# Kernel tuning notes

Hardware: AMD Instinct MI355X
Metric: run time of the kernel (lower is better)

Reference implementation:

```python
import jax, jax.numpy as jnp
import numpy as np
import math

DIM = 1024
H = 16
HD = DIM // H  # 64
M = 64         # num_features
B, S = 4, 4096


def setup_inputs() -> dict:
    key = jax.random.key(0)
    ks = jax.random.split(key, 10)
    sc = 1.0 / math.sqrt(DIM)
    return {
        "x": jax.random.normal(ks[0], (B, S, DIM), dtype=jnp.float32),
        "Wq": jax.random.normal(ks[1], (DIM, DIM), dtype=jnp.float32) * sc,
        "bq": jax.random.normal(ks[2], (DIM,), dtype=jnp.float32) * 0.01,
        "Wk": jax.random.normal(ks[3], (DIM, DIM), dtype=jnp.float32) * sc,
        "bk": jax.random.normal(ks[4], (DIM,), dtype=jnp.float32) * 0.01,
        "Wv": jax.random.normal(ks[5], (DIM, DIM), dtype=jnp.float32) * sc,
        "bv": jax.random.normal(ks[6], (DIM,), dtype=jnp.float32) * 0.01,
        "Wo": jax.random.normal(ks[7], (DIM, DIM), dtype=jnp.float32) * sc,
        "bo": jax.random.normal(ks[8], (DIM,), dtype=jnp.float32) * 0.01,
        "P": jax.random.normal(ks[9], (H, M, HD), dtype=jnp.float32),
    }


def _feature_map(t, P):
    # t: [b,h,s,d], P: [h,m,d] -> relu(t @ P^T) / sqrt(m)
    proj = jnp.einsum("bhsd,hmd->bhsm", t, P)
    return jax.nn.relu(proj) * (1.0 / math.sqrt(P.shape[1]))


def reference(x, Wq, bq, Wk, bk, Wv, bv, Wo, bo, P):
    b, s, dim = x.shape
    h, m, hd = P.shape
    # Linear projections (torch Linear: x @ W^T + b), split heads -> [b,h,s,hd]
    def split_heads(y):
        return y.reshape(b, s, h, hd).transpose(0, 2, 1, 3)
    q = split_heads(x @ Wq.T + bq)
    k = split_heads(x @ Wk.T + bk)
    v = split_heads(x @ Wv.T + bv)
    q_prime = _feature_map(q, P)  # [b,h,s,m]
    k_prime = _feature_map(k, P)  # [b,h,s,m]
    kv = jnp.einsum("bhsm,bhsd->bhmd", k_prime, v)       # [b,h,m,hd]
    attn = jnp.einsum("bhsm,bhmd->bhsd", q_prime, kv)    # [b,h,s,hd]
    attn = attn.transpose(0, 2, 1, 3).reshape(b, s, dim)
    return attn @ Wo.T + bo
```

## Files before the change

kernel.cpp:

```cpp
#include <hip/hip_runtime.h>
#include <hip/hip_bf16.h>
#include <cstdint>

typedef __bf16 bf16_t;
typedef bf16_t bf16x8 __attribute__((ext_vector_type(8)));
typedef float f32x4 __attribute__((ext_vector_type(4)));
typedef float f32x16 __attribute__((ext_vector_type(16)));


__device__ __forceinline__ void gload_lds16(const bf16_t* g, bf16_t* l) {
  __builtin_amdgcn_global_load_lds(
      (const __attribute__((address_space(1))) uint32_t*)g,
      (__attribute__((address_space(3))) uint32_t*)l, 16, 0, 0);
}

__global__ void prep_misc(const float* __restrict__ x, const float* __restrict__ Wv,
                          const float* __restrict__ bv,
                          bf16_t* __restrict__ xb, bf16_t* __restrict__ WvO,
                          float* __restrict__ bcat) {
  int b = blockIdx.x, t = threadIdx.x;
  if (b < 8192) {
    long i = (long)b * 256 + t;
    const f32x4* p = (const f32x4*)(x + i * 8);
    f32x4 a = p[0], c = p[1];
    bf16x8 o;
#pragma unroll
    for (int j = 0; j < 4; ++j) { o[j] = (bf16_t)a[j]; o[j + 4] = (bf16_t)c[j]; }
    *(bf16x8*)(xb + i * 8) = o;
  } else if (b < 8704) {
    long i = (long)(b - 8192) * 256 + t;
    const f32x4* p = (const f32x4*)(Wv + i * 8);
    f32x4 a = p[0], c = p[1];
    bf16x8 o;
#pragma unroll
    for (int j = 0; j < 4; ++j) { o[j] = (bf16_t)a[j]; o[j + 4] = (bf16_t)c[j]; }
    *(bf16x8*)(WvO + i * 8) = o;
  } else {
    *(f32x4*)&bcat[2048 + t * 4] = *(const f32x4*)&bv[t * 4];
  }
}

__global__ __launch_bounds__(256) void prep_wqk(
    const float* __restrict__ Wq, const float* __restrict__ bq,
    const float* __restrict__ Wk, const float* __restrict__ bk,
    const float* __restrict__ P,
    bf16_t* __restrict__ Wcat, float* __restrict__ bcat)
{
  int bid = blockIdx.x;
  int qk = bid >> 7, h = (bid >> 3) & 15, kt = bid & 7;
  const float* W = qk ? Wk : Wq;
  const float* bias = qk ? bk : bq;
  __shared__ float Pl[64 * 64];
  __shared__ float Wlt[128 * 68];
  int t = threadIdx.x;
  int k0 = kt * 128;
  for (int i = t * 4; i < 4096; i += 1024)
    *(f32x4*)&Pl[i] = *(const f32x4*)&P[h * 4096 + i];
  for (int fi = t; fi < 2048; fi += 256) {
    int row = fi >> 5;
    int c4 = fi & 31;
    f32x4 w = *(const f32x4*)&W[(long)(h * 64 + row) * 1024 + k0 + c4 * 4];
#pragma unroll
    for (int j = 0; j < 4; ++j) Wlt[(c4 * 4 + j) * 68 + row] = w[j];
  }
  __syncthreads();
  int kloc = t >> 1;
  int mh = (t & 1) * 32;
  for (int m = mh; m < mh + 32; ++m) {
    f32x4 s = {0.f, 0.f, 0.f, 0.f};
#pragma unroll
    for (int dd = 0; dd < 16; ++dd)
      s += (*(const f32x4*)&Pl[m * 64 + dd * 4]) * (*(const f32x4*)&Wlt[kloc * 68 + dd * 4]);
    float a = s[0] + s[1] + s[2] + s[3];
    Wcat[(long)(qk * 1024 + h * 64 + m) * 1024 + k0 + kloc] = (bf16_t)a;
  }
  if (kt == 0 && t < 64) {
    float a = 0.f;
    for (int d = 0; d < 64; ++d) a += Pl[t * 64 + d] * bias[h * 64 + d];
    bcat[qk * 1024 + h * 64 + t] = a;
  }
}

template <int EPI>
__global__ __launch_bounds__(512, 2) void gemm256(
    const bf16_t* __restrict__ A, int lda,
    const bf16_t* __restrict__ B0, int ldb,
    const float* __restrict__ bias,
    void* __restrict__ Cv, int ldc,
    int K, int ncols, int cpx,
    int rows_per_batch, long bstride)
{
  __shared__ bf16_t sA[2][16384];
  __shared__ bf16_t sB[2][16384];

  const int lin = blockIdx.x;
  const int wgid = (lin & 7) * cpx + (lin >> 3);
  const int row0 = (wgid / ncols) * 256;
  const int col0 = (wgid % ncols) * 256;

  const int tid = threadIdx.x;
  const int w = tid >> 6, l = tid & 63;
  const int wr = w >> 2, wc = w & 3;
  const int l31 = l & 31, kh = l >> 5, x7 = l & 7;

  const bf16_t* Bm = B0 + (long)(row0 / rows_per_batch) * bstride;

  long a_off[4], b_off[4];
#pragma unroll
  for (int i = 0; i < 4; ++i) {
    int c = i * 512 + tid;
    int r = c >> 3;
    int kqs = (c & 7) ^ (r & 7);
    a_off[i] = (long)(row0 + r) * lda + kqs * 8;
    b_off[i] = (long)(col0 + r) * ldb + kqs * 8;
  }
  const int ldst = tid * 8;

  const int abase = (wr * 128 + l31) * 64;
  const int bbase = (wc * 64 + l31) * 64;
  const int e0 = ((0 + kh) ^ x7) * 8;
  const int e1 = ((2 + kh) ^ x7) * 8;
  const int e2 = ((4 + kh) ^ x7) * 8;
  const int e3 = ((6 + kh) ^ x7) * 8;

  f32x16 acc[4][2] = {};
  const int NT = K >> 6;

#pragma unroll
  for (int i = 0; i < 4; ++i) {
    gload_lds16(A + a_off[i], &sA[0][i * 4096 + ldst]);
    gload_lds16(Bm + b_off[i], &sB[0][i * 4096 + ldst]);
  }
  __syncthreads();

#define TILE_BODY(PC, PN, T)                                                            \
  {                                                                                     \
    bf16x8 afr[4][2], bfr[2][2];                                                        \
    _Pragma("unroll") for (int mi = 0; mi < 4; ++mi) {                                  \
      afr[mi][0] = *(const bf16x8*)&sA[PC][abase + mi * 2048 + e0];                     \
      afr[mi][1] = *(const bf16x8*)&sA[PC][abase + mi * 2048 + e1];                     \
    }                                                                                   \
    _Pragma("unroll") for (int ni = 0; ni < 2; ++ni) {                                  \
      bfr[ni][0] = *(const bf16x8*)&sB[PC][bbase + ni * 2048 + e0];                     \
      bfr[ni][1] = *(const bf16x8*)&sB[PC][bbase + ni * 2048 + e1];                     \
    }                                                                                   \
    if ((T) + 1 < NT) {                                                                 \
      long ks = (long)((T) + 1) * 64;                                                   \
      _Pragma("unroll") for (int i = 0; i < 4; ++i) {                                   \
        gload_lds16(A + a_off[i] + ks, &sA[PN][i * 4096 + ldst]);                       \
        gload_lds16(Bm + b_off[i] + ks, &sB[PN][i * 4096 + ldst]);                      \
      }                                                                                 \
    }                                                                                   \
    __builtin_amdgcn_s_setprio(1);                                                      \
    _Pragma("unroll") for (int mi = 0; mi < 4; ++mi)                                    \
      _Pragma("unroll") for (int ni = 0; ni < 2; ++ni) {                                \
        acc[mi][ni] = __builtin_amdgcn_mfma_f32_32x32x16_bf16(afr[mi][0], bfr[ni][0], acc[mi][ni], 0, 0, 0); \
        acc[mi][ni] = __builtin_amdgcn_mfma_f32_32x32x16_bf16(afr[mi][1], bfr[ni][1], acc[mi][ni], 0, 0, 0); \
      }                                                                                 \
    __builtin_amdgcn_s_setprio(0);                                                      \
    _Pragma("unroll") for (int mi = 0; mi < 4; ++mi) {                                  \
      afr[mi][0] = *(const bf16x8*)&sA[PC][abase + mi * 2048 + e2];                     \
      afr[mi][1] = *(const bf16x8*)&sA[PC][abase + mi * 2048 + e3];                     \
    }                                                                                   \
    _Pragma("unroll") for (int ni = 0; ni < 2; ++ni) {                                  \
      bfr[ni][0] = *(const bf16x8*)&sB[PC][bbase + ni * 2048 + e2];                     \
      bfr[ni][1] = *(const bf16x8*)&sB[PC][bbase + ni * 2048 + e3];                     \
    }                                                                                   \
    __builtin_amdgcn_s_setprio(1);                                                      \
    _Pragma("unroll") for (int mi = 0; mi < 4; ++mi)                                    \
      _Pragma("unroll") for (int ni = 0; ni < 2; ++ni) {                                \
        acc[mi][ni] = __builtin_amdgcn_mfma_f32_32x32x16_bf16(afr[mi][0], bfr[ni][0], acc[mi][ni], 0, 0, 0); \
        acc[mi][ni] = __builtin_amdgcn_mfma_f32_32x32x16_bf16(afr[mi][1], bfr[ni][1], acc[mi][ni], 0, 0, 0); \
      }                                                                                 \
    __builtin_amdgcn_s_setprio(0);                                                      \
    __syncthreads();                                                                    \
  }

  for (int t = 0; t < NT; t += 2) {
    TILE_BODY(0, 1, t);
    TILE_BODY(1, 0, t + 1);
  }
#undef TILE_BODY

#pragma unroll
  for (int ni = 0; ni < 2; ++ni) {
    const int gcol = col0 + wc * 64 + ni * 32 + l31;
    const float bz = bias[gcol];
    const bool doRelu = (EPI == 1) && (gcol < 2048);
#pragma unroll
    for (int mi = 0; mi < 4; ++mi) {
      const int rbase = row0 + wr * 128 + mi * 32 + 4 * kh;
#pragma unroll
      for (int reg = 0; reg < 16; ++reg) {
        const int grow = rbase + (reg & 3) + 8 * (reg >> 2);
        float v = acc[mi][ni][reg] + bz;
        if constexpr (EPI == 1) { if (doRelu) v = fmaxf(v, 0.f) * 0.125f; }
        if constexpr (EPI == 2)
          ((float*)Cv)[(long)grow * ldc + gcol] = v;
        else
          ((bf16_t*)Cv)[(long)grow * ldc + gcol] = (bf16_t)v;
      }
    }
  }
}

__global__ __launch_bounds__(512, 4) void gemm128(
    const bf16_t* __restrict__ A, int lda,
    const bf16_t* __restrict__ B0, int ldb,
    const float* __restrict__ bias,
    float* __restrict__ C, int ldc,
    int K, int ncols, int cpx,
    int rows_per_batch, long bstride)
{
  __shared__ bf16_t sA[2][8192];
  __shared__ bf16_t sB[2][8192];

  const int lin = blockIdx.x;
  const int wgid = (lin & 7) * cpx + (lin >> 3);
  const int row0 = (wgid / ncols) * 128;
  const int col0 = (wgid % ncols) * 128;

  const int tid = threadIdx.x;
  const int w = tid >> 6, l = tid & 63;
  const int wr = w >> 2, wc = w & 3;
  const int l31 = l & 31, kh = l >> 5, x7 = l & 7;

  const bf16_t* Bm = B0 + (long)(row0 / rows_per_batch) * bstride;

  long a_off[2], b_off[2];
#pragma unroll
  for (int i = 0; i < 2; ++i) {
    int c = i * 512 + tid;
    int r = c >> 3;
    int kqs = (c & 7) ^ (r & 7);
    a_off[i] = (long)(row0 + r) * lda + kqs * 8;
    b_off[i] = (long)(col0 + r) * ldb + kqs * 8;
  }
  const int ldst = tid * 8;

  const int abase = (wr * 64 + l31) * 64;
  const int bbase = (wc * 32 + l31) * 64;
  const int e0 = ((0 + kh) ^ x7) * 8;
  const int e1 = ((2 + kh) ^ x7) * 8;
  const int e2 = ((4 + kh) ^ x7) * 8;
  const int e3 = ((6 + kh) ^ x7) * 8;

  f32x16 acc[2] = {};
  const int NT = K >> 6;

#pragma unroll
  for (int i = 0; i < 2; ++i) {
    gload_lds16(A + a_off[i], &sA[0][i * 4096 + ldst]);
    gload_lds16(Bm + b_off[i], &sB[0][i * 4096 + ldst]);
  }
  __syncthreads();

#define TILE128(PC, PN, T)                                                              \
  {                                                                                     \
    bf16x8 afr[2][2], bfr[2];                                                           \
    _Pragma("unroll") for (int mi = 0; mi < 2; ++mi) {                                  \
      afr[mi][0] = *(const bf16x8*)&sA[PC][abase + mi * 2048 + e0];                     \
      afr[mi][1] = *(const bf16x8*)&sA[PC][abase + mi * 2048 + e1];                     \
    }                                                                                   \
    bfr[0] = *(const bf16x8*)&sB[PC][bbase + e0];                                       \
    bfr[1] = *(const bf16x8*)&sB[PC][bbase + e1];                                       \
    if ((T) + 1 < NT) {                                                                 \
      long ks = (long)((T) + 1) * 64;                                                   \
      _Pragma("unroll") for (int i = 0; i < 2; ++i) {                                   \
        gload_lds16(A + a_off[i] + ks, &sA[PN][i * 4096 + ldst]);                       \
        gload_lds16(Bm + b_off[i] + ks, &sB[PN][i * 4096 + ldst]);                      \
      }                                                                                 \
    }                                                                                   \
    __builtin_amdgcn_s_setprio(1);                                                      \
    _Pragma("unroll") for (int mi = 0; mi < 2; ++mi) {                                  \
      acc[mi] = __builtin_amdgcn_mfma_f32_32x32x16_bf16(afr[mi][0], bfr[0], acc[mi], 0, 0, 0); \
      acc[mi] = __builtin_amdgcn_mfma_f32_32x32x16_bf16(afr[mi][1], bfr[1], acc[mi], 0, 0, 0); \
    }                                                                                   \
    __builtin_amdgcn_s_setprio(0);                                                      \
    _Pragma("unroll") for (int mi = 0; mi < 2; ++mi) {                                  \
      afr[mi][0] = *(const bf16x8*)&sA[PC][abase + mi * 2048 + e2];                     \
      afr[mi][1] = *(const bf16x8*)&sA[PC][abase + mi * 2048 + e3];                     \
    }                                                                                   \
    bfr[0] = *(const bf16x8*)&sB[PC][bbase + e2];                                       \
    bfr[1] = *(const bf16x8*)&sB[PC][bbase + e3];                                       \
    __builtin_amdgcn_s_setprio(1);                                                      \
    _Pragma("unroll") for (int mi = 0; mi < 2; ++mi) {                                  \
      acc[mi] = __builtin_amdgcn_mfma_f32_32x32x16_bf16(afr[mi][0], bfr[0], acc[mi], 0, 0, 0); \
      acc[mi] = __builtin_amdgcn_mfma_f32_32x32x16_bf16(afr[mi][1], bfr[1], acc[mi], 0, 0, 0); \
    }                                                                                   \
    __builtin_amdgcn_s_setprio(0);                                                      \
    __syncthreads();                                                                    \
  }

  for (int t = 0; t < NT; t += 2) {
    TILE128(0, 1, t);
    TILE128(1, 0, t + 1);
  }
#undef TILE128

  const int gcol = col0 + wc * 32 + l31;
  const float bz = bias[gcol];
#pragma unroll
  for (int mi = 0; mi < 2; ++mi) {
    const int rbase = row0 + wr * 64 + mi * 32 + 4 * kh;
#pragma unroll
    for (int reg = 0; reg < 16; ++reg) {
      const int grow = rbase + (reg & 3) + 8 * (reg >> 2);
      C[(long)grow * ldc + gcol] = acc[mi][reg] + bz;
    }
  }
}

__global__ __launch_bounds__(256) void kv_partial(
    const bf16_t* __restrict__ QKV, float* __restrict__ kvpart)
{
  int bh = blockIdx.x;
  int split = blockIdx.y;
  int b = bh >> 4, h = bh & 15;
  __shared__ alignas(16) bf16_t Kt[64 * 32];
  __shared__ alignas(16) bf16_t Vt[64 * 32];
  int t = threadIdx.x;
  int wv = t >> 6, lane = t & 63, lhi = lane >> 4, llo = lane & 15;
  int r = t >> 3;
  int c = (t & 7) * 8;
  f32x4 acc[4] = {};
  long rowbase = ((long)b * 4096 + split * 512) * 3072 + h * 64 + c;
  for (int sc = 0; sc < 16; ++sc) {
    long off = rowbase + (long)(sc * 32 + r) * 3072;
    bf16x8 kk = *(const bf16x8*)(QKV + off + 1024);
    bf16x8 vvv = *(const bf16x8*)(QKV + off + 2048);
#pragma unroll
    for (int j = 0; j < 8; ++j) {
      Kt[(c + j) * 32 + r] = kk[j];
      Vt[(c + j) * 32 + r] = vvv[j];
    }
    __syncthreads();
    bf16x8 a = *(const bf16x8*)&Kt[(wv * 16 + llo) * 32 + lhi * 8];
#pragma unroll
    for (int ni = 0; ni < 4; ++ni) {
      bf16x8 bb = *(const bf16x8*)&Vt[(ni * 16 + llo) * 32 + lhi * 8];
      acc[ni] = __builtin_amdgcn_mfma_f32_16x16x32_bf16(a, bb, acc[ni], 0, 0, 0);
    }
    __syncthreads();
  }
#pragma unroll
  for (int ni = 0; ni < 4; ++ni)
#pragma unroll
    for (int j = 0; j < 4; ++j) {
      int m = wv * 16 + lhi * 4 + j;
      int d = ni * 16 + llo;
      kvpart[((long)split * 64 + bh) * 4096 + m * 64 + d] = acc[ni][j];
    }
}

__global__ void kv_reduce(const float* __restrict__ part, float* __restrict__ kv) {
  int i = blockIdx.x * 256 + threadIdx.x;
  float s = 0.f;
#pragma unroll
  for (int sp = 0; sp < 8; ++sp) s += part[sp * 262144 + i];
  kv[i] = s;
}

__global__ __launch_bounds__(256) void wcombt_kernel(
    const float* __restrict__ kv, const float* __restrict__ Wo,
    bf16_t* __restrict__ WcT)
{
  int nt = blockIdx.x, h = blockIdx.y, b = blockIdx.z;
  __shared__ float kvs[4096];
  int t = threadIdx.x;
  for (int i = t * 4; i < 4096; i += 1024)
    *(f32x4*)&kvs[i] = *(const f32x4*)&kv[((long)b * 16 + h) * 4096 + i];
  __syncthreads();
  int n = nt * 128 + (t >> 1);
  int mh = (t & 1) * 32;
  f32x4 wo[16];
#pragma unroll
  for (int dd = 0; dd < 16; ++dd) wo[dd] = *(const f32x4*)&Wo[(long)n * 1024 + h * 64 + dd * 4];
  for (int m = mh; m < mh + 32; ++m) {
    f32x4 s = {0.f, 0.f, 0.f, 0.f};
#pragma unroll
    for (int dd = 0; dd < 16; ++dd)
      s += (*(const f32x4*)&kvs[m * 64 + dd * 4]) * wo[dd];
    WcT[((long)b * 1024 + n) * 1024 + h * 64 + m] = (bf16_t)(s[0] + s[1] + s[2] + s[3]);
  }
}

extern "C" void kernel_launch(void* const* d_in, const int* in_sizes, int n_in,
                              void* d_out, int out_size, void* d_ws, size_t ws_size,
                              hipStream_t stream) {
  (void)in_sizes; (void)n_in; (void)out_size; (void)ws_size;
  const float* x  = (const float*)d_in[0];
  const float* Wq = (const float*)d_in[1];
  const float* bq = (const float*)d_in[2];
  const float* Wk = (const float*)d_in[3];
  const float* bk = (const float*)d_in[4];
  const float* Wv = (const float*)d_in[5];
  const float* bv = (const float*)d_in[6];
  const float* Wo = (const float*)d_in[7];
  const float* bo = (const float*)d_in[8];
  const float* P  = (const float*)d_in[9];
  float* out = (float*)d_out;

  char* ws = (char*)d_ws;
  bf16_t* xb     = (bf16_t*)(ws + 0);
  bf16_t* QKV    = (bf16_t*)(ws + 33554432);
  bf16_t* Wcat   = (bf16_t*)(ws + 134217728);
  float*  bcat   = (float*) (ws + 140509184);
  float*  kvpart = (float*) (ws + 140521472);
  float*  kvbuf  = (float*) (ws + 148910080);
  bf16_t* WcT    = (bf16_t*)(ws + 149958656);

  prep_misc<<<8705, 256, 0, stream>>>(x, Wv, bv, xb, Wcat + (size_t)2048 * 1024, bcat);
  prep_wqk<<<256, 256, 0, stream>>>(Wq, bq, Wk, bk, P, Wcat, bcat);

  gemm256<1><<<768, 512, 0, stream>>>(
      xb, 1024, Wcat, 1024, bcat, QKV, 3072, 1024, 12, 96, 1 << 30, 0);

  kv_partial<<<dim3(64, 8), 256, 0, stream>>>(QKV, kvpart);
  kv_reduce<<<1024, 256, 0, stream>>>(kvpart, kvbuf);

  wcombt_kernel<<<dim3(8, 16, 4), 256, 0, stream>>>(kvbuf, Wo, WcT);

  gemm128<<<1024, 512, 0, stream>>>(
      QKV, 3072, WcT, 1024, bo, out, 1024, 1024, 8, 128, 4096, (long)1024 * 1024);
}
```

Before: 232.4 us.

## Store LDS tiles in MFMA fragment order instead of XOR-swizzled rows

Both GEMM kernels now stage global tiles into shared memory so that each wave's MFMA operand fragment is a contiguous 64-lane run of 16-byte chunks. The per-lane XOR swizzle and its address arithmetic go away, and LDS reads become linear, conflict-free vector loads. The cost moves to global loads: each thread now fetches 16-byte pieces spread across rows with strided k offsets, which may reduce coalescing per wavefront.

```diff
diff --git a/kernel.cpp b/kernel.cpp
--- a/kernel.cpp
+++ b/kernel.cpp
@@ -101,27 +101,30 @@
   const int tid = threadIdx.x;
   const int w = tid >> 6, l = tid & 63;
   const int wr = w >> 2, wc = w & 3;
-  const int l31 = l & 31, kh = l >> 5, x7 = l & 7;
+  const int l31 = l & 31, kh = l >> 5;
+  const int lofs = l * 8;
 
   const bf16_t* Bm = B0 + (long)(row0 / rows_per_batch) * bstride;
 
   long a_off[4], b_off[4];
 #pragma unroll
-  for (int i = 0; i < 4; ++i) {
-    int c = i * 512 + tid;
-    int r = c >> 3;
-    int kqs = (c & 7) ^ (r & 7);
-    a_off[i] = (long)(row0 + r) * lda + kqs * 8;
-    b_off[i] = (long)(col0 + r) * ldb + kqs * 8;
+  for (int j = 0; j < 4; ++j) {
+    int c = j * 512 + tid;
+    int h = c >> 10;
+    int cr = c & 1023;
+    int s = cr >> 8;
+    int mi = (cr >> 6) & 3;
+    int khs = (cr >> 5) & 1;
+    int r31 = cr & 31;
+    int row = h * 128 + mi * 32 + r31;
+    int kk = s * 16 + khs * 8;
+    a_off[j] = (long)(row0 + row) * lda + kk;
+    b_off[j] = (long)(col0 + row) * ldb + kk;
   }
   const int ldst = tid * 8;
 
-  const int abase = (wr * 128 + l31) * 64;
-  const int bbase = (wc * 64 + l31) * 64;
-  const int e0 = ((0 + kh) ^ x7) * 8;
-  const int e1 = ((2 + kh) ^ x7) * 8;
-  const int e2 = ((4 + kh) ^ x7) * 8;
-  const int e3 = ((6 + kh) ^ x7) * 8;
+  const int abase = wr * 8192 + lofs;
+  const int bbase = (wc >> 1) * 8192 + (wc & 1) * 1024 + lofs;
 
   f32x16 acc[4][2] = {};
   const int NT = K >> 6;
@@ -137,12 +140,12 @@
   {                                                                                     \
     bf16x8 afr[4][2], bfr[2][2];                                                        \
     _Pragma("unroll") for (int mi = 0; mi < 4; ++mi) {                                  \
-      afr[mi][0] = *(const bf16x8*)&sA[PC][abase + mi * 2048 + e0];                     \
-      afr[mi][1] = *(const bf16x8*)&sA[PC][abase + mi * 2048 + e1];                     \
+      afr[mi][0] = *(const bf16x8*)&sA[PC][abase + mi * 512];                           \
+      afr[mi][1] = *(const bf16x8*)&sA[PC][abase + 2048 + mi * 512];                    \
     }                                                                                   \
     _Pragma("unroll") for (int ni = 0; ni < 2; ++ni) {                                  \
-      bfr[ni][0] = *(const bf16x8*)&sB[PC][bbase + ni * 2048 + e0];                     \
-      bfr[ni][1] = *(const bf16x8*)&sB[PC][bbase + ni * 2048 + e1];                     \
+      bfr[ni][0] = *(const bf16x8*)&sB[PC][bbase + ni * 512];                           \
+      bfr[ni][1] = *(const bf16x8*)&sB[PC][bbase + 2048 + ni * 512];                    \
     }                                                                                   \
     if ((T) + 1 < NT) {                                                                 \
       long ks = (long)((T) + 1) * 64;                                                   \
@@ -159,12 +162,12 @@
       }                                                                                 \
     __builtin_amdgcn_s_setprio(0);                                                      \
     _Pragma("unroll") for (int mi = 0; mi < 4; ++mi) {                                  \
-      afr[mi][0] = *(const bf16x8*)&sA[PC][abase + mi * 2048 + e2];                     \
-      afr[mi][1] = *(const bf16x8*)&sA[PC][abase + mi * 2048 + e3];                     \
+      afr[mi][0] = *(const bf16x8*)&sA[PC][abase + 4096 + mi * 512];                    \
+      afr[mi][1] = *(const bf16x8*)&sA[PC][abase + 6144 + mi * 512];                    \
     }                                                                                   \
     _Pragma("unroll") for (int ni = 0; ni < 2; ++ni) {                                  \
-      bfr[ni][0] = *(const bf16x8*)&sB[PC][bbase + ni * 2048 + e2];                     \
-      bfr[ni][1] = *(const bf16x8*)&sB[PC][bbase + ni * 2048 + e3];                     \
+      bfr[ni][0] = *(const bf16x8*)&sB[PC][bbase + 4096 + ni * 512];                    \
+      bfr[ni][1] = *(const bf16x8*)&sB[PC][bbase + 6144 + ni * 512];                    \
     }                                                                                   \
     __builtin_amdgcn_s_setprio(1);                                                      \
     _Pragma("unroll") for (int mi = 0; mi < 4; ++mi)                                    \
@@ -223,27 +226,28 @@
   const int tid = threadIdx.x;
   const int w = tid >> 6, l = tid & 63;
   const int wr = w >> 2, wc = w & 3;
-  const int l31 = l & 31, kh = l >> 5, x7 = l & 7;
+  const int l31 = l & 31, kh = l >> 5;
+  const int lofs = l * 8;
 
   const bf16_t* Bm = B0 + (long)(row0 / rows_per_batch) * bstride;
 
   long a_off[2], b_off[2];
 #pragma unroll
-  for (int i = 0; i < 2; ++i) {
-    int c = i * 512 + tid;
-    int r = c >> 3;
-    int kqs = (c & 7) ^ (r & 7);
-    a_off[i] = (long)(row0 + r) * lda + kqs * 8;
-    b_off[i] = (long)(col0 + r) * ldb + kqs * 8;
+  for (int j = 0; j < 2; ++j) {
+    int c = j * 512 + tid;
+    int s = c >> 8;
+    int mi = (c >> 6) & 3;
+    int khs = (c >> 5) & 1;
+    int r31 = c & 31;
+    int row = mi * 32 + r31;
+    int kk = s * 16 + khs * 8;
+    a_off[j] = (long)(row0 + row) * lda + kk;
+    b_off[j] = (long)(col0 + row) * ldb + kk;
   }
   const int ldst = tid * 8;
 
-  const int abase = (wr * 64 + l31) * 64;
-  const int bbase = (wc * 32 + l31) * 64;
-  const int e0 = ((0 + kh) ^ x7) * 8;
-  const int e1 = ((2 + kh) ^ x7) * 8;
-  const int e2 = ((4 + kh) ^ x7) * 8;
-  const int e3 = ((6 + kh) ^ x7) * 8;
+  const int abase = wr * 1024 + lofs;
+  const int bbase = wc * 512 + lofs;
 
   f32x16 acc[2] = {};
   const int NT = K >> 6;
@@ -259,11 +263,11 @@
   {                                                                                     \
     bf16x8 afr[2][2], bfr[2];                                                           \
     _Pragma("unroll") for (int mi = 0; mi < 2; ++mi) {                                  \
-      afr[mi][0] = *(const bf16x8*)&sA[PC][abase + mi * 2048 + e0];                     \
-      afr[mi][1] = *(const bf16x8*)&sA[PC][abase + mi * 2048 + e1];                     \
-    }                                                                                   \
-    bfr[0] = *(const bf16x8*)&sB[PC][bbase + e0];                                       \
-    bfr[1] = *(const bf16x8*)&sB[PC][bbase + e1];                                       \
+      afr[mi][0] = *(const bf16x8*)&sA[PC][abase + mi * 512];                           \
+      afr[mi][1] = *(const bf16x8*)&sA[PC][abase + 2048 + mi * 512];                    \
+    }                                                                                   \
+    bfr[0] = *(const bf16x8*)&sB[PC][bbase];                                            \
+    bfr[1] = *(const bf16x8*)&sB[PC][bbase + 2048];                                     \
     if ((T) + 1 < NT) {                                                                 \
       long ks = (long)((T) + 1) * 64;                                                   \
       _Pragma("unroll") for (int i = 0; i < 2; ++i) {                                   \
@@ -278,11 +282,11 @@
     }                                                                                   \
     __builtin_amdgcn_s_setprio(0);                                                      \
     _Pragma("unroll") for (int mi = 0; mi < 2; ++mi) {                                  \
-      afr[mi][0] = *(const bf16x8*)&sA[PC][abase + mi * 2048 + e2];                     \
-      afr[mi][1] = *(const bf16x8*)&sA[PC][abase + mi * 2048 + e3];                     \
-    }                                                                                   \
-    bfr[0] = *(const bf16x8*)&sB[PC][bbase + e2];                                       \
-    bfr[1] = *(const bf16x8*)&sB[PC][bbase + e3];                                       \
+      afr[mi][0] = *(const bf16x8*)&sA[PC][abase + 4096 + mi * 512];                    \
+      afr[mi][1] = *(const bf16x8*)&sA[PC][abase + 6144 + mi * 512];                    \
+    }                                                                                   \
+    bfr[0] = *(const bf16x8*)&sB[PC][bbase + 4096];                                     \
+    bfr[1] = *(const bf16x8*)&sB[PC][bbase + 6144];                                     \
     __builtin_amdgcn_s_setprio(1);                                                      \
     _Pragma("unroll") for (int mi = 0; mi < 2; ++mi) {                                  \
       acc[mi] = __builtin_amdgcn_mfma_f32_32x32x16_bf16(afr[mi][0], bfr[0], acc[mi], 0, 0, 0); \
```

Measured after the change: 294.3 us. +26.6%, slower.
